# Kernel tuning notes

Hardware: AMD Instinct MI355X
Metric: run time of the kernel (lower is better)

Reference implementation:

```python
import jax, jax.numpy as jnp
import numpy as np

B, S, D = 4, 2048, 1024
H, DK, DV = 16, 64, 64
NEG = -1e10


def setup_inputs() -> dict:
    key = jax.random.key(0)
    ks = jax.random.split(key, 7)
    queries = jax.random.normal(ks[0], (B, S, D), dtype=jnp.float32)
    keys = jax.random.normal(ks[1], (B, S, D), dtype=jnp.float32)
    values = jax.random.normal(ks[2], (B, S, D), dtype=jnp.float32)
    mask = jnp.ones((B, S, S), dtype=jnp.int32)
    # per-head Linear weights, torch layout [out, in]; stacked over heads
    Wq = jax.random.normal(ks[3], (H, DK, D), dtype=jnp.float32) / np.sqrt(D)
    Wk = jax.random.normal(ks[4], (H, DK, D), dtype=jnp.float32) / np.sqrt(D)
    Wv = jax.random.normal(ks[5], (H, DV, D), dtype=jnp.float32) / np.sqrt(D)
    Wo = jax.random.normal(ks[6], (D, H * DV), dtype=jnp.float32) / np.sqrt(H * DV)
    return {"queries": queries, "keys": keys, "values": values, "mask": mask,
            "Wq": Wq, "Wk": Wk, "Wv": Wv, "Wo": Wo}


def reference(queries, keys, values, mask, Wq, Wk, Wv, Wo):
    # per-head projections, vectorized over heads: y = x @ W_h^T
    q = jnp.einsum('bsd,hkd->bhsk', queries, Wq)   # [B,H,S,DK]
    k = jnp.einsum('btd,hkd->bhtk', keys, Wk)      # [B,H,S,DK]
    v = jnp.einsum('btd,hvd->bhtv', values, Wv)    # [B,H,S,DV]
    scores = jnp.einsum('bhsk,bhtk->bhst', q, k) / jnp.sqrt(jnp.asarray(DK, q.dtype))
    scores = jnp.where(mask[:, None, :, :] == 0, jnp.asarray(NEG, q.dtype), scores)
    attn = jax.nn.softmax(scores, axis=-1)
    out = jnp.einsum('bhst,bhtv->bhsv', attn, v)   # [B,H,S,DV]
    # torch.cat over heads on last dim == head-major concat per position
    out = out.transpose(0, 2, 1, 3).reshape(B, S, H * DV)
    return out @ Wo.T
```

## Files before the change

### kernel.cpp

```cpp
#include <hip/hip_runtime.h>
#include <stdint.h>

typedef __attribute__((ext_vector_type(4))) float f32x4;
typedef __attribute__((ext_vector_type(8))) __bf16 bf16x8;
typedef __attribute__((ext_vector_type(4))) __bf16 bf16x4;
typedef __attribute__((ext_vector_type(4))) short s16x4;
typedef __attribute__((ext_vector_type(2))) uint32_t u32x2;

#define MFMA16(a, b, c) __builtin_amdgcn_mfma_f32_16x16x32_bf16(a, b, c, 0, 0, 0)
#define MFMA16K16(a, b, c) __builtin_amdgcn_mfma_f32_16x16x16bf16_1k(a, b, c, 0, 0, 0)

#define B_ 4
#define S_ 2048
#define D_ 1024
#define H_ 16
#define NEG_ -1e10f
#define QSCALE 0.180336880f
#define MNEG_ -100.0f

__device__ __forceinline__ float ex2(float x) { return __builtin_amdgcn_exp2f(x); }

__device__ __forceinline__ void glds16(const void* gsrc, void* ldst) {
  __builtin_amdgcn_global_load_lds(
      (__attribute__((address_space(1))) void*)(gsrc),
      (__attribute__((address_space(3))) void*)(ldst),
      16, 0, 0);
}

__device__ __forceinline__ uint32_t pack_bf16(float a, float b) {
  uint32_t ua = (uint32_t)__builtin_bit_cast(unsigned short, (__bf16)a);
  uint32_t ub = (uint32_t)__builtin_bit_cast(unsigned short, (__bf16)b);
  return ua | (ub << 16);
}

__global__ __launch_bounds__(256) void prep(
    const float* __restrict__ xq, const float* __restrict__ xk, const float* __restrict__ xv,
    const float* __restrict__ wq, const float* __restrict__ wk, const float* __restrict__ wv,
    const float* __restrict__ wo,
    __bf16* __restrict__ oxq, __bf16* __restrict__ oxk, __bf16* __restrict__ oxv,
    __bf16* __restrict__ owq, __bf16* __restrict__ owk, __bf16* __restrict__ owv,
    __bf16* __restrict__ owo,
    const int* __restrict__ mask, uint32_t* __restrict__ bits, int* __restrict__ flags) {
  int bid = blockIdx.x, tid = threadIdx.x;
  __shared__ int andred;
  if (bid < 24576) {
    int z = bid >> 13, xb = bid & 8191;
    const float* in = (z == 0) ? xq : (z == 1) ? xk : xv;
    __bf16* out = (z == 0) ? oxq : (z == 1) ? oxk : oxv;
    int i = (xb * 256 + tid) * 4;
    float4 v = *(const float4*)(in + i);
    bf16x4 o;
    o.x = (__bf16)v.x; o.y = (__bf16)v.y; o.z = (__bf16)v.z; o.w = (__bf16)v.w;
    *(bf16x4*)(out + i) = o;
  } else if (bid < 28672) {
    int m = bid - 24576;
    int z = m >> 10, wb = m & 1023;
    const float* in = (z == 0) ? wq : (z == 1) ? wk : (z == 2) ? wv : wo;
    __bf16* out = (z == 0) ? owq : (z == 1) ? owk : (z == 2) ? owv : owo;
    int i = (wb * 256 + tid) * 4;
    float4 v = *(const float4*)(in + i);
    bf16x4 o;
    o.x = (__bf16)v.x; o.y = (__bf16)v.y; o.z = (__bf16)v.z; o.w = (__bf16)v.w;
    *(bf16x4*)(out + i) = o;
  } else {
    int m = bid - 28672;
    int tt = m & 15, st = (m >> 4) & 15, b = m >> 8;
    int w = tid >> 6, lane = tid & 63;
    if (tid == 0) andred = 1;
    __syncthreads();
    unsigned long long all1 = ~0ull;
    for (int rr = 0; rr < 32; rr++) {
      int srow = st * 128 + w * 32 + rr;
      #pragma unroll
      for (int half = 0; half < 2; half++) {
        int c = tt * 128 + half * 64 + lane;
        int mm = mask[((size_t)b * S_ + srow) * S_ + c];
        unsigned long long bal = __ballot(mm != 0);
        all1 &= bal;
        if (lane == 0) {
          uint32_t* dst = &bits[((size_t)b * S_ + srow) * 64 + tt * 4 + half * 2];
          dst[0] = (uint32_t)bal;
          dst[1] = (uint32_t)(bal >> 32);
        }
      }
    }
    if (all1 != ~0ull) atomicAnd(&andred, 0);
    __syncthreads();
    if (tid == 0) flags[(b * 16 + st) * 16 + tt] = andred;
  }
}

template <int MODE>
__global__ __launch_bounds__(256, 3) void gemm_bt(
    const __bf16* __restrict__ A0, const __bf16* __restrict__ A1, const __bf16* __restrict__ A2,
    const __bf16* __restrict__ W0, const __bf16* __restrict__ W1, const __bf16* __restrict__ W2,
    void* O0, void* O1, void* O2) {
  const int K = 1024;
  int lin = blockIdx.y * 8 + blockIdx.x;
  int swz = (lin & 7) * 64 + (lin >> 3);
  int bx = swz & 7, by = swz >> 3;

  const __bf16* PA; const __bf16* PB; void* O;
  int pa_t, pb_t;
  if (MODE == 0) {
    if (blockIdx.z == 0)      { PA = W0; PB = A0; O = O0; pa_t = bx; pb_t = by; }
    else if (blockIdx.z == 1) { PA = W1; PB = A1; O = O1; pa_t = bx; pb_t = by; }
    else                      { PA = A2; PB = W2; O = O2; pa_t = by; pb_t = bx; }
  } else { PA = W0; PB = A0; O = O0; pa_t = bx; pb_t = by; }

  __shared__ __align__(16) __bf16 As[128 * 64];
  __shared__ __align__(16) __bf16 Bs[128 * 64];
  int tid = threadIdx.x, lane = tid & 63, w = tid >> 6;
  int wm = w >> 1, wn = w & 1;
  int g = lane >> 4, l15 = lane & 15;
  f32x4 acc[4][4] = {};
  const __bf16* Ablk = PA + (size_t)(pa_t * 128) * K;
  const __bf16* Bblk = PB + (size_t)(pb_t * 128) * K;

  for (int kt = 0; kt < K; kt += 64) {
    __syncthreads();
    #pragma unroll
    for (int r = 0; r < 4; r++) {
      int C = r * 256 + tid;
      int row = C >> 3, c = C & 7;
      int c0 = c ^ (row & 7);
      glds16(Ablk + (size_t)row * K + kt + c0 * 8, (char*)As + C * 16);
      glds16(Bblk + (size_t)row * K + kt + c0 * 8, (char*)Bs + C * 16);
    }
    __syncthreads();
    #pragma unroll
    for (int kkq = 0; kkq < 2; kkq++) {
      bf16x8 af[4], bfr[4];
      #pragma unroll
      for (int i = 0; i < 4; i++) {
        int row = wm * 64 + i * 16 + l15;
        int ch = (kkq * 4 + g) ^ (row & 7);
        af[i] = *(const bf16x8*)((const char*)As + row * 128 + ch * 16);
      }
      #pragma unroll
      for (int j = 0; j < 4; j++) {
        int row = wn * 64 + j * 16 + l15;
        int ch = (kkq * 4 + g) ^ (row & 7);
        bfr[j] = *(const bf16x8*)((const char*)Bs + row * 128 + ch * 16);
      }
      #pragma unroll
      for (int i = 0; i < 4; i++)
        #pragma unroll
        for (int j = 0; j < 4; j++)
          acc[i][j] = MFMA16(af[i], bfr[j], acc[i][j]);
    }
  }

  if (MODE == 1) {
    #pragma unroll
    for (int i = 0; i < 4; i++)
      #pragma unroll
      for (int j = 0; j < 4; j++) {
        int n0 = pa_t * 128 + wm * 64 + i * 16 + g * 4;
        int m = pb_t * 128 + wn * 64 + j * 16 + l15;
        *(f32x4*)((float*)O + (size_t)m * 1024 + n0) = acc[i][j];
      }
  } else if (blockIdx.z == 2) {
    #pragma unroll
    for (int i = 0; i < 4; i++)
      #pragma unroll
      for (int j = 0; j < 4; j++) {
        int s0 = pa_t * 128 + wm * 64 + i * 16 + g * 4;
        int dvg = pb_t * 128 + wn * 64 + j * 16 + l15;
        int b = s0 >> 11, s = s0 & 2047;
        int h = dvg >> 6, dv = dvg & 63;
        bf16x4 o;
        #pragma unroll
        for (int r = 0; r < 4; r++) o[r] = (__bf16)acc[i][j][r];
        *(bf16x4*)((__bf16*)O + (((size_t)b * 16 + h) * 64 + dv) * 2048 + s) = o;
      }
  } else {
    float scale = (blockIdx.z == 0) ? QSCALE : 1.0f;
    #pragma unroll
    for (int i = 0; i < 4; i++)
      #pragma unroll
      for (int j = 0; j < 4; j++) {
        int dkg = pa_t * 128 + wm * 64 + i * 16 + g * 4;
        int sg = pb_t * 128 + wn * 64 + j * 16 + l15;
        int h = dkg >> 6, dk = dkg & 63;
        int b = sg >> 11, s = sg & 2047;
        bf16x4 o;
        #pragma unroll
        for (int r = 0; r < 4; r++) o[r] = (__bf16)(acc[i][j][r] * scale);
        *(bf16x4*)((__bf16*)O + (((size_t)b * 16 + h) * 2048 + s) * 64 + dk) = o;
      }
  }
}

__global__ __launch_bounds__(256, 4) void attn(
    const __bf16* __restrict__ qp, const __bf16* __restrict__ kp,
    const __bf16* __restrict__ vt_, __bf16* __restrict__ aout,
    const uint32_t* __restrict__ bits, const int* __restrict__ flags) {
  int lin = blockIdx.y * 16 + blockIdx.x;
  int swz = (lin & 7) * 128 + (lin >> 3);
  int qt = swz & 15, bh = swz >> 4;
  int b = bh >> 4, h = bh & 15;
  int tid = threadIdx.x, lane = tid & 63, w = tid >> 6;
  int g = lane >> 4, l15 = lane & 15;
  int hs0 = ((g & 1) ^ ((l15 >> 3) & 1)) * 8;

  __shared__ __align__(16) char smem[32768];

  const __bf16* Qg = qp + ((size_t)bh * S_ + qt * 128) * 64;
  const __bf16* Kg = kp + (size_t)bh * S_ * 64;
  const __bf16* Vg = vt_ + (size_t)bh * 64 * S_;

  #pragma unroll
  for (int r = 0; r < 4; r++) {
    int C = r * 256 + tid;
    int row = C >> 3, c = C & 7, c0 = c ^ (row & 7);
    glds16(Qg + row * 64 + c0 * 8, smem + C * 16);
  }
  __syncthreads();
  bf16x8 qf[2][2];
  #pragma unroll
  for (int i = 0; i < 2; i++)
    #pragma unroll
    for (int kkq = 0; kkq < 2; kkq++) {
      int row = w * 32 + i * 16 + l15;
      int ch = (kkq * 4 + g) ^ (row & 7);
      qf[i][kkq] = *(const bf16x8*)(smem + row * 128 + ch * 16);
    }
  __syncthreads();

  auto stageK = [&](int kt2, int p) {
    char* Kl = smem + p * 16384;
    const __bf16* Ks = Kg + (size_t)kt2 * 64 * 64;
    #pragma unroll
    for (int r = 0; r < 2; r++) {
      int C = r * 256 + tid;
      int row = C >> 3, c = C & 7, c0 = c ^ (row & 7);
      glds16(Ks + (size_t)row * 64 + c0 * 8, Kl + C * 16);
    }
  };
  auto loadV = [&](int kt2, int4* vreg) {
    #pragma unroll
    for (int r = 0; r < 2; r++) {
      int C = r * 256 + tid;
      int row = C >> 3, c = C & 7;
      int c0 = c ^ (row & 7);
      vreg[r] = *(const int4*)(Vg + (size_t)row * S_ + kt2 * 64 + c0 * 8);
    }
  };
  auto writeV = [&](int p, const int4* vreg) {
    char* Vl = smem + p * 16384 + 8192;
    #pragma unroll
    for (int r = 0; r < 2; r++) {
      int C = r * 256 + tid;
      int row = C >> 3;
      int4 v = vreg[r];
      bool sw = (row & 8) != 0;
      int4 wv;
      wv.x = sw ? v.z : v.x; wv.y = sw ? v.w : v.y;
      wv.z = sw ? v.x : v.z; wv.w = sw ? v.y : v.w;
      *(int4*)(Vl + C * 16) = wv;
    }
  };

  f32x4 oacc[4][2] = {};
  f32x4 sumacc[2] = {};
  const f32x4 zero4 = {0.f, 0.f, 0.f, 0.f};
  const s16x4 ones = {(short)0x3F80, (short)0x3F80, (short)0x3F80, (short)0x3F80};

  int4 vreg[2];

  stageK(0, 0);
  loadV(0, vreg);
  asm volatile("s_waitcnt vmcnt(0)" ::: "memory");
  writeV(0, vreg);
  asm volatile("s_waitcnt lgkmcnt(0)" ::: "memory");
  __builtin_amdgcn_s_barrier();
  __builtin_amdgcn_sched_barrier(0);

  for (int kt = 0; kt < 32; kt++) {
    int cur = kt & 1;
    if (kt + 1 < 32) {
      stageK(kt + 1, cur ^ 1);
      loadV(kt + 1, vreg);
    }
    __builtin_amdgcn_sched_barrier(0);

    const char* Klds = smem + cur * 16384;
    const char* Vlds = Klds + 8192;
    int fl = flags[(b * 16 + qt) * 16 + (kt >> 1)];

    f32x4 sacc[2][4];
    __builtin_amdgcn_s_setprio(1);
    #pragma unroll
    for (int jt = 0; jt < 4; jt++) {
      int row = jt * 16 + l15;
      bf16x8 kf0 = *(const bf16x8*)(Klds + row * 128 + (g ^ (row & 7)) * 16);
      bf16x8 kf1 = *(const bf16x8*)(Klds + row * 128 + ((4 + g) ^ (row & 7)) * 16);
      sacc[0][jt] = MFMA16(kf0, qf[0][0], zero4);
      sacc[0][jt] = MFMA16(kf1, qf[0][1], sacc[0][jt]);
      sacc[1][jt] = MFMA16(kf0, qf[1][0], zero4);
      sacc[1][jt] = MFMA16(kf1, qf[1][1], sacc[1][jt]);
    }
    __builtin_amdgcn_s_setprio(0);

    if (!fl) {
      #pragma unroll
      for (int i = 0; i < 2; i++) {
        int srow = qt * 128 + w * 32 + i * 16 + l15;
        const uint32_t* bw = &bits[((size_t)b * S_ + srow) * 64 + kt * 2];
        uint32_t mw[2] = {bw[0], bw[1]};
        #pragma unroll
        for (int jt = 0; jt < 4; jt++)
          #pragma unroll
          for (int r = 0; r < 4; r++) {
            int bitpos = (jt & 1) * 16 + g * 4 + r;
            if (!((mw[jt >> 1] >> bitpos) & 1)) sacc[i][jt][r] = MNEG_;
          }
      }
    }

    #pragma unroll
    for (int jt = 0; jt < 4; jt++) {
      s16x4 pf[2];
      #pragma unroll
      for (int i = 0; i < 2; i++) {
        float p0 = ex2(sacc[i][jt][0]);
        float p1 = ex2(sacc[i][jt][1]);
        float p2 = ex2(sacc[i][jt][2]);
        float p3 = ex2(sacc[i][jt][3]);
        u32x2 t;
        t.x = pack_bf16(p0, p1);
        t.y = pack_bf16(p2, p3);
        pf[i] = __builtin_bit_cast(s16x4, t);
      }
      int ch = jt * 2 + (g >> 1);
      __builtin_amdgcn_s_setprio(1);
      #pragma unroll
      for (int vt = 0; vt < 4; vt++) {
        int row = vt * 16 + l15;
        int chs = ch ^ (row & 7);
        s16x4 vv = *(const s16x4*)(Vlds + row * 128 + chs * 16 + hs0);
        oacc[vt][0] = MFMA16K16(vv, pf[0], oacc[vt][0]);
        oacc[vt][1] = MFMA16K16(vv, pf[1], oacc[vt][1]);
      }
      sumacc[0] = MFMA16K16(ones, pf[0], sumacc[0]);
      sumacc[1] = MFMA16K16(ones, pf[1], sumacc[1]);
      __builtin_amdgcn_s_setprio(0);
    }

    asm volatile("s_waitcnt vmcnt(0)" ::: "memory");
    if (kt + 1 < 32) writeV(cur ^ 1, vreg);
    asm volatile("s_waitcnt lgkmcnt(0)" ::: "memory");
    __builtin_amdgcn_s_barrier();
    __builtin_amdgcn_sched_barrier(0);
  }

  #pragma unroll
  for (int i = 0; i < 2; i++) {
    float inv = 1.0f / sumacc[i][0];
    int srow = qt * 128 + w * 32 + i * 16 + l15;
    #pragma unroll
    for (int vt = 0; vt < 4; vt++) {
      bf16x4 o;
      #pragma unroll
      for (int r = 0; r < 4; r++) o[r] = (__bf16)(oacc[vt][i][r] * inv);
      *(bf16x4*)(aout + ((size_t)b * S_ + srow) * 1024 + h * 64 + vt * 16 + g * 4) = o;
    }
  }
}

extern "C" void kernel_launch(void* const* d_in, const int* in_sizes, int n_in,
                              void* d_out, int out_size, void* d_ws, size_t ws_size,
                              hipStream_t stream) {
  const float* queries = (const float*)d_in[0];
  const float* keys    = (const float*)d_in[1];
  const float* values  = (const float*)d_in[2];
  const int*   mask    = (const int*)d_in[3];
  const float* Wq      = (const float*)d_in[4];
  const float* Wk      = (const float*)d_in[5];
  const float* Wv      = (const float*)d_in[6];
  const float* Wo      = (const float*)d_in[7];

  char* ws = (char*)d_ws;
  __bf16* Xq  = (__bf16*)(ws + 0);
  __bf16* Xk  = (__bf16*)(ws + 16777216);
  __bf16* Xv  = (__bf16*)(ws + 33554432);
  __bf16* Wqb = (__bf16*)(ws + 50331648);
  __bf16* Wkb = (__bf16*)(ws + 52428800);
  __bf16* Wvb = (__bf16*)(ws + 54525952);
  __bf16* Wob = (__bf16*)(ws + 56623104);
  __bf16* qp  = (__bf16*)(ws + 58720256);
  __bf16* kp  = (__bf16*)(ws + 75497472);
  __bf16* vT  = (__bf16*)(ws + 92274688);
  uint32_t* bits = (uint32_t*)(ws + 109051904);
  int* flags     = (int*)(ws + 111149056);
  __bf16* aout = Xq;

  prep<<<29696, 256, 0, stream>>>(queries, keys, values, Wq, Wk, Wv, Wo,
                                  Xq, Xk, Xv, Wqb, Wkb, Wvb, Wob,
                                  mask, bits, flags);

  gemm_bt<0><<<dim3(8, 64, 3), 256, 0, stream>>>(Xq, Xk, Xv, Wqb, Wkb, Wvb,
                                                 (void*)qp, (void*)kp, (void*)vT);

  attn<<<dim3(16, 64), 256, 0, stream>>>(qp, kp, vT, aout, bits, flags);

  gemm_bt<1><<<dim3(8, 64, 1), 256, 0, stream>>>(aout, nullptr, nullptr, Wob, nullptr, nullptr,
                                                 (void*)d_out, nullptr, nullptr);
}
```

Measured before the change: 404.5 us.

## Coarsen prep conversion blocks and vectorize mask bit-packing per thread

```diff
diff --git a/kernel.cpp b/kernel.cpp
--- a/kernel.cpp
+++ b/kernel.cpp
@@ -42,51 +42,49 @@
     __bf16* __restrict__ owo,
     const int* __restrict__ mask, uint32_t* __restrict__ bits, int* __restrict__ flags) {
   int bid = blockIdx.x, tid = threadIdx.x;
-  __shared__ int andred;
-  if (bid < 24576) {
-    int z = bid >> 13, xb = bid & 8191;
+  if (bid < 1536) {
+    int z = bid >> 9, local = bid & 511;
     const float* in = (z == 0) ? xq : (z == 1) ? xk : xv;
     __bf16* out = (z == 0) ? oxq : (z == 1) ? oxk : oxv;
-    int i = (xb * 256 + tid) * 4;
-    float4 v = *(const float4*)(in + i);
-    bf16x4 o;
-    o.x = (__bf16)v.x; o.y = (__bf16)v.y; o.z = (__bf16)v.z; o.w = (__bf16)v.w;
-    *(bf16x4*)(out + i) = o;
-  } else if (bid < 28672) {
-    int m = bid - 24576;
-    int z = m >> 10, wb = m & 1023;
+    #pragma unroll
+    for (int it = 0; it < 16; it++) {
+      size_t i4 = (size_t)(local * 256 + tid) + (size_t)it * (512 * 256);
+      float4 v = *(const float4*)(in + i4 * 4);
+      bf16x4 o;
+      o.x = (__bf16)v.x; o.y = (__bf16)v.y; o.z = (__bf16)v.z; o.w = (__bf16)v.w;
+      *(bf16x4*)(out + i4 * 4) = o;
+    }
+  } else if (bid < 1792) {
+    int m = bid - 1536;
+    int z = m >> 6, local = m & 63;
     const float* in = (z == 0) ? wq : (z == 1) ? wk : (z == 2) ? wv : wo;
     __bf16* out = (z == 0) ? owq : (z == 1) ? owk : (z == 2) ? owv : owo;
-    int i = (wb * 256 + tid) * 4;
-    float4 v = *(const float4*)(in + i);
-    bf16x4 o;
-    o.x = (__bf16)v.x; o.y = (__bf16)v.y; o.z = (__bf16)v.z; o.w = (__bf16)v.w;
-    *(bf16x4*)(out + i) = o;
+    #pragma unroll
+    for (int it = 0; it < 16; it++) {
+      size_t i4 = (size_t)(local * 256 + tid) + (size_t)it * (64 * 256);
+      float4 v = *(const float4*)(in + i4 * 4);
+      bf16x4 o;
+      o.x = (__bf16)v.x; o.y = (__bf16)v.y; o.z = (__bf16)v.z; o.w = (__bf16)v.w;
+      *(bf16x4*)(out + i4 * 4) = o;
+    }
   } else {
-    int m = bid - 28672;
-    int tt = m & 15, st = (m >> 4) & 15, b = m >> 8;
-    int w = tid >> 6, lane = tid & 63;
-    if (tid == 0) andred = 1;
-    __syncthreads();
-    unsigned long long all1 = ~0ull;
-    for (int rr = 0; rr < 32; rr++) {
-      int srow = st * 128 + w * 32 + rr;
-      #pragma unroll
-      for (int half = 0; half < 2; half++) {
-        int c = tt * 128 + half * 64 + lane;
-        int mm = mask[((size_t)b * S_ + srow) * S_ + c];
-        unsigned long long bal = __ballot(mm != 0);
-        all1 &= bal;
-        if (lane == 0) {
-          uint32_t* dst = &bits[((size_t)b * S_ + srow) * 64 + tt * 4 + half * 2];
-          dst[0] = (uint32_t)bal;
-          dst[1] = (uint32_t)(bal >> 32);
-        }
-      }
-    }
-    if (all1 != ~0ull) atomicAnd(&andred, 0);
-    __syncthreads();
-    if (tid == 0) flags[(b * 16 + st) * 16 + tt] = andred;
+    int wid = (bid - 1792) * 256 + tid;
+    int word = wid & 63, grow = wid >> 6;
+    const int* mp = mask + (size_t)grow * S_ + word * 32;
+    uint32_t wbits = 0;
+    #pragma unroll
+    for (int j = 0; j < 8; j++) {
+      int4 mv = *(const int4*)(mp + j * 4);
+      wbits |= (mv.x != 0 ? 1u : 0u) << (j * 4);
+      wbits |= (mv.y != 0 ? 1u : 0u) << (j * 4 + 1);
+      wbits |= (mv.z != 0 ? 1u : 0u) << (j * 4 + 2);
+      wbits |= (mv.w != 0 ? 1u : 0u) << (j * 4 + 3);
+    }
+    bits[(size_t)grow * 64 + word] = wbits;
+    if (wbits != 0xFFFFFFFFu) {
+      int b = grow >> 11, srow = grow & 2047;
+      atomicAnd(&flags[(b * 16 + (srow >> 7)) * 16 + (word >> 2)], 0);
+    }
   }
 }
 
@@ -396,9 +394,11 @@
   int* flags     = (int*)(ws + 111149056);
   __bf16* aout = Xq;
 
-  prep<<<29696, 256, 0, stream>>>(queries, keys, values, Wq, Wk, Wv, Wo,
-                                  Xq, Xk, Xv, Wqb, Wkb, Wvb, Wob,
-                                  mask, bits, flags);
+  hipMemsetAsync(flags, 0xFF, 4096, stream);
+
+  prep<<<3840, 256, 0, stream>>>(queries, keys, values, Wq, Wk, Wv, Wo,
+                                 Xq, Xk, Xv, Wqb, Wkb, Wvb, Wob,
+                                 mask, bits, flags);
 
   gemm_bt<0><<<dim3(8, 64, 3), 256, 0, stream>>>(Xq, Xk, Xv, Wqb, Wkb, Wvb,
                                                  (void*)qp, (void*)kp, (void*)vT);
```

Result: faster. 384.4 us (-5.0%).
